# Kernel tuning notes

Hardware: AMD Instinct MI355X
Metric: run time of the kernel (lower is better)

Reference implementation:

```python
import jax, jax.numpy as jnp
import numpy as np

B, S, D = 2, 2048, 512
P, T, MAP_H = 13, 5, 64


def setup_inputs() -> dict:
    key = jax.random.key(0)
    ks = jax.random.split(key, 8)
    s = 0.02
    return {
        "hidden_states": jax.random.normal(ks[0], (B, S, D), jnp.float32),
        "ln_gamma": jnp.ones((D,), jnp.float32),
        "ln_beta": jnp.zeros((D,), jnp.float32),
        "W_in": jax.random.normal(ks[1], (D, P * D), jnp.float32) * s,
        "b_in": jnp.zeros((P * D,), jnp.float32),
        "W_map1": jax.random.normal(ks[2], (D, MAP_H), jnp.float32) * s,
        "b_map1": jnp.zeros((MAP_H,), jnp.float32),
        "W_map2": jax.random.normal(ks[3], (MAP_H, T), jnp.float32) * s,
        "b_map2": jnp.zeros((T,), jnp.float32),
        "log_tau": jnp.linspace(0.0, 4.0, T).astype(jnp.float32),
        "mix": jax.random.normal(ks[4], (P, T), jnp.float32) / float(P * T),
        "W_out": jax.random.normal(ks[5], (D, D), jnp.float32) * s,
        "b_out": jnp.zeros((D,), jnp.float32),
        "scale": jnp.float32(1e-3),
        "h_prev": jnp.zeros((B, P, T, D), jnp.float32),
        "position_offset": 0,
    }


def _forward(hidden_states, ln_gamma, ln_beta, W_in, b_in, W_map1, b_map1,
             W_map2, b_map2, log_tau, mix, W_out, b_out, scale, h_prev):
    b, s_len, d = hidden_states.shape
    p, t = mix.shape
    # pre-norm (LayerNorm, eps=1e-5)
    mu = jnp.mean(hidden_states, -1, keepdims=True)
    var = jnp.var(hidden_states, -1, keepdims=True)
    xn = (hidden_states - mu) * jax.lax.rsqrt(var + 1e-5) * ln_gamma + ln_beta
    # per-protofilament input drive: [B,S,P,D]
    u = (xn @ W_in + b_in).reshape(b, s_len, p, d)
    # liquid (input-dependent) decay per time scale: [B,S,T]
    gate = jax.nn.sigmoid(jnp.tanh(xn @ W_map1 + b_map1) @ W_map2 + b_map2)
    alpha = jnp.exp(-gate / jnp.exp(log_tau))  # [B,S,T]

    def step(h, inp):
        u_t, a_t = inp                      # [B,P,D], [B,T]
        a = a_t[:, None, :, None]           # broadcast over P and D
        h = a * h + (1.0 - a) * u_t[:, :, None, :]   # [B,P,T,D]
        y = jnp.einsum('bptd,pt->bd', h, mix)        # mix protofilaments/time scales
        return h, y

    _, ys = jax.lax.scan(step, h_prev,
                         (jnp.moveaxis(u, 1, 0), jnp.moveaxis(alpha, 1, 0)))
    mt_out = jnp.moveaxis(ys, 0, 1) @ W_out + b_out  # [B,S,D]
    return hidden_states + scale * mt_out


def reference(hidden_states, ln_gamma, ln_beta, W_in, b_in, W_map1, b_map1,
              W_map2, b_map2, log_tau, mix, W_out, b_out, scale, h_prev,
              position_offset):
    return _forward(hidden_states, ln_gamma, ln_beta, W_in, b_in, W_map1,
                    b_map1, W_map2, b_map2, log_tau, mix, W_out, b_out,
                    scale, h_prev)
```

## Files before the change

kernel.cpp:

```cpp
#include <hip/hip_runtime.h>
#include <hip/hip_bf16.h>
#include <stdint.h>

#define BB 2
#define SS 2048
#define DD 512
#define PP 13
#define TT 5
#define MH 64
#define MM (BB*SS)
#define NV (TT*DD)
#define KK 512
#define CHUNK 16
#define NCH (SS/CHUNK)

typedef __attribute__((ext_vector_type(4))) float f32x4;
typedef __attribute__((ext_vector_type(8))) short s8v;
typedef unsigned int u32;
typedef __attribute__((address_space(3))) u32 lds_u32_t;
typedef __attribute__((address_space(1))) const u32 glb_u32_t;

__device__ __forceinline__ float bf2f(unsigned short u){
  union { unsigned int i; float f; } c; c.i = ((unsigned int)u) << 16; return c.f;
}
__device__ __forceinline__ unsigned short f2bf(float f){
  union { float f; unsigned int i; } c; c.f = f;
  unsigned int x = c.i;
  unsigned int r = (x + 0x7fffu + ((x >> 16) & 1u)) >> 16;
  return (unsigned short)r;
}
__device__ __forceinline__ void gld16(unsigned short* l, const unsigned short* g){
  __builtin_amdgcn_global_load_lds((glb_u32_t*)g, (lds_u32_t*)l, 16, 0, 0);
}

__global__ __launch_bounds__(256) void k_prep(
    const float* __restrict__ W_in, const float* __restrict__ b_in,
    const float* __restrict__ mix,  const float* __restrict__ W_out,
    const float* __restrict__ W1,
    unsigned short* __restrict__ W_vT, float* __restrict__ b_v,
    unsigned short* __restrict__ W_outT, unsigned short* __restrict__ W1T)
{
  int blk = blockIdx.x;
  if (blk < 128){
    int idx = blk * 256 + threadIdx.x;
    int d  = idx & (DD-1);
    int k0 = idx >> 9;
    float mx[PP][TT];
    #pragma unroll
    for (int p=0;p<PP;++p)
      #pragma unroll
      for (int t=0;t<TT;++t) mx[p][t] = mix[p*TT+t];
    float acc[TT][8];
    #pragma unroll
    for (int t=0;t<TT;++t)
      #pragma unroll
      for (int j=0;j<8;++j) acc[t][j] = 0.f;
    #pragma unroll
    for (int j=0;j<8;++j){
      int k = k0*8 + j;
      const float* wrow = W_in + (size_t)k * (PP*DD) + d;
      #pragma unroll
      for (int p=0;p<PP;++p){
        float w = wrow[p*DD];
        #pragma unroll
        for (int t=0;t<TT;++t) acc[t][j] += mx[p][t]*w;
      }
    }
    #pragma unroll
    for (int t=0;t<TT;++t){
      union { unsigned short us[8]; uint4 u; } pk;
      #pragma unroll
      for (int j=0;j<8;++j) pk.us[j] = f2bf(acc[t][j]);
      *(uint4*)(W_vT + ((size_t)(t*DD+d))*KK + k0*8) = pk.u;
    }
    if (k0 == 0){
      #pragma unroll
      for (int t=0;t<TT;++t){
        float s = 0.f;
        #pragma unroll
        for (int p=0;p<PP;++p) s += mx[p][t]*b_in[p*DD+d];
        b_v[t*DD+d] = s;
      }
    }
  } else if (blk < 256){
    int idx = (blk-128)*256 + threadIdx.x;
    int n  = idx & (DD-1);
    int k0 = idx >> 9;
    union { unsigned short us[8]; uint4 u; } pk;
    #pragma unroll
    for (int j=0;j<8;++j) pk.us[j] = f2bf(W_out[(size_t)(k0*8+j)*DD + n]);
    *(uint4*)(W_outT + (size_t)n*KK + k0*8) = pk.u;
  } else {
    int idx = (blk-256)*256 + threadIdx.x;
    int n  = idx >> 6;
    int k0 = idx & 63;
    union { unsigned short us[8]; uint4 u; } pk;
    #pragma unroll
    for (int j=0;j<8;++j) pk.us[j] = f2bf(W1[(size_t)(k0*8+j)*MH + n]);
    *(uint4*)(W1T + (size_t)n*KK + k0*8) = pk.u;
  }
}

__global__ __launch_bounds__(256) void k_ln(
    const float* __restrict__ hs,
    const float* __restrict__ gamma, const float* __restrict__ beta,
    unsigned short* __restrict__ xn_bf)
{
  int tid = threadIdx.x;
  int lane = tid & 63;
  int row = blockIdx.x*4 + (tid>>6);
  const float* x = hs + (size_t)row*DD + lane*8;
  float4 v0 = *(const float4*)x;
  float4 v1 = *(const float4*)(x+4);
  float s  = v0.x+v0.y+v0.z+v0.w + v1.x+v1.y+v1.z+v1.w;
  float sq = v0.x*v0.x+v0.y*v0.y+v0.z*v0.z+v0.w*v0.w
           + v1.x*v1.x+v1.y*v1.y+v1.z*v1.z+v1.w*v1.w;
  #pragma unroll
  for (int o=32;o>0;o>>=1){ s += __shfl_xor(s,o); sq += __shfl_xor(sq,o); }
  float mu   = s  * (1.f/DD);
  float var  = sq * (1.f/DD) - mu*mu;
  float rstd = rsqrtf(var + 1e-5f);
  float4 g0 = *(const float4*)(gamma + lane*8);
  float4 g1 = *(const float4*)(gamma + lane*8 + 4);
  float4 b0 = *(const float4*)(beta  + lane*8);
  float4 b1 = *(const float4*)(beta  + lane*8 + 4);
  union { unsigned short us[8]; uint4 u; } pk;
  pk.us[0] = f2bf((v0.x-mu)*rstd*g0.x + b0.x);
  pk.us[1] = f2bf((v0.y-mu)*rstd*g0.y + b0.y);
  pk.us[2] = f2bf((v0.z-mu)*rstd*g0.z + b0.z);
  pk.us[3] = f2bf((v0.w-mu)*rstd*g0.w + b0.w);
  pk.us[4] = f2bf((v1.x-mu)*rstd*g1.x + b1.x);
  pk.us[5] = f2bf((v1.y-mu)*rstd*g1.y + b1.y);
  pk.us[6] = f2bf((v1.z-mu)*rstd*g1.z + b1.z);
  pk.us[7] = f2bf((v1.w-mu)*rstd*g1.w + b1.w);
  *(uint4*)(xn_bf + (size_t)row*DD + lane*8) = pk.u;
}

__global__ __launch_bounds__(256) void k_gate(
    const unsigned short* __restrict__ xn,
    const unsigned short* __restrict__ W1T,
    const float* __restrict__ b1, const float* __restrict__ W2,
    const float* __restrict__ b2, const float* __restrict__ ltau,
    float* __restrict__ alpha)
{
  __shared__ unsigned short lA[2][64*32];
  __shared__ unsigned short lB[2][64*32];
  int bm = blockIdx.x;
  int tid = threadIdx.x, lane = tid & 63, w = tid >> 6;
  int lr = lane & 15, kq = lane >> 4;
  const uint8_t* gA = (const uint8_t*)(xn  + (size_t)(bm*64 + w*16 + (lane>>2))*KK) + (lane&3)*16;
  const uint8_t* gB = (const uint8_t*)(W1T + (size_t)(        w*16 + (lane>>2))*KK) + (lane&3)*16;
  f32x4 acc[4];
  #pragma unroll
  for (int ni=0;ni<4;++ni) acc[ni] = (f32x4){0.f,0.f,0.f,0.f};

  auto stage = [&](int buf, int kt){
    int off = kt*64;
    gld16(&lA[buf][(w*16)*32], (const unsigned short*)(gA + off));
    gld16(&lB[buf][(w*16)*32], (const unsigned short*)(gB + off));
  };
  auto compute = [&](int buf){
    union { uint4 u; s8v v; } af, bfr[4];
    af.u = *(const uint4*)&lA[buf][(w*16+lr)*32 + kq*8];
    #pragma unroll
    for (int ni=0;ni<4;++ni) bfr[ni].u = *(const uint4*)&lB[buf][(ni*16+lr)*32 + kq*8];
    #pragma unroll
    for (int ni=0;ni<4;++ni)
      acc[ni] = __builtin_amdgcn_mfma_f32_16x16x32_bf16(af.v, bfr[ni].v, acc[ni], 0,0,0);
  };

  stage(0, 0);
  __syncthreads();
  #pragma unroll
  for (int kt=1; kt<16; ++kt){
    stage(kt&1, kt);
    compute((kt&1)^1);
    __syncthreads();
  }
  compute(1);

  float z1[4][4];
  #pragma unroll
  for (int ni=0;ni<4;++ni){
    float bb = b1[ni*16+lr];
    #pragma unroll
    for (int r=0;r<4;++r) z1[r][ni] = tanhf(acc[ni][r] + bb);
  }
  float et[TT];
  #pragma unroll
  for (int t=0;t<TT;++t) et[t] = expf(-ltau[t]);
  float a[4][TT];
  #pragma unroll
  for (int t=0;t<TT;++t){
    float w2[4];
    #pragma unroll
    for (int ni=0;ni<4;++ni) w2[ni] = W2[(ni*16+lr)*TT + t];
    #pragma unroll
    for (int r=0;r<4;++r){
      float p = z1[r][0]*w2[0] + z1[r][1]*w2[1] + z1[r][2]*w2[2] + z1[r][3]*w2[3];
      #pragma unroll
      for (int o=8;o>0;o>>=1) p += __shfl_xor(p, o);
      float z2 = p + b2[t];
      float gate = 1.f/(1.f + expf(-z2));
      a[r][t] = expf(-gate * et[t]);
    }
  }
  if (lr < TT){
    int t = lr;
    #pragma unroll
    for (int r=0;r<4;++r){
      int row = bm*64 + w*16 + kq*4 + r;
      alpha[(size_t)row*TT + t] = a[r][t];
    }
  }
}

template<int BN, int NDIM, bool OUTEPI>
__global__ __launch_bounds__(256) void k_gemm(
    const unsigned short* __restrict__ A,
    const unsigned short* __restrict__ Bt,
    const float* __restrict__ bias,
    const float* __restrict__ hidden,
    const float* __restrict__ scale_p,
    float* __restrict__ outF,
    unsigned short* __restrict__ outBf)
{
  constexpr int NI  = (BN == 128) ? 4 : 2;
  constexpr int WNT = BN / 2;
  __shared__ unsigned short lA[2][128*32];
  __shared__ unsigned short lB[2][BN*32];
  int bn = blockIdx.x, bm = blockIdx.y;
  int tid  = threadIdx.x;
  int lane = tid & 63;
  int w    = tid >> 6;
  int wm = w >> 1, wn = w & 1;
  f32x4 acc[4][NI];
  #pragma unroll
  for (int i=0;i<4;++i)
    #pragma unroll
    for (int j=0;j<NI;++j) acc[i][j] = (f32x4){0.f,0.f,0.f,0.f};

  const uint8_t* gA = (const uint8_t*)(A + (size_t)(bm*128 + w*32 + (lane>>2))*KK) + (lane&3)*16;
  const uint8_t* gB;
  if constexpr (BN == 128) gB = (const uint8_t*)(Bt + (size_t)(bn*BN + w*32 + (lane>>2))*KK) + (lane&3)*16;
  else                     gB = (const uint8_t*)(Bt + (size_t)(bn*BN + w*16 + (lane>>2))*KK) + (lane&3)*16;
  int lr = lane & 15, kq = lane >> 4;

  auto stage = [&](int buf, int kt){
    int off = kt*64;
    gld16(&lA[buf][(w*32)*32],    (const unsigned short*)(gA + off));
    gld16(&lA[buf][(w*32+16)*32], (const unsigned short*)(gA + (size_t)16*KK*2 + off));
    if constexpr (BN == 128){
      gld16(&lB[buf][(w*32)*32],    (const unsigned short*)(gB + off));
      gld16(&lB[buf][(w*32+16)*32], (const unsigned short*)(gB + (size_t)16*KK*2 + off));
    } else {
      gld16(&lB[buf][(w*16)*32],    (const unsigned short*)(gB + off));
    }
  };
  auto compute = [&](int buf){
    union { uint4 u; s8v v; } af[4], bfr[NI];
    #pragma unroll
    for (int mi=0;mi<4;++mi) af[mi].u  = *(const uint4*)&lA[buf][(wm*64+mi*16+lr)*32 + kq*8];
    #pragma unroll
    for (int ni=0;ni<NI;++ni) bfr[ni].u = *(const uint4*)&lB[buf][(wn*WNT+ni*16+lr)*32 + kq*8];
    #pragma unroll
    for (int mi=0;mi<4;++mi)
      #pragma unroll
      for (int ni=0;ni<NI;++ni)
        acc[mi][ni] = __builtin_amdgcn_mfma_f32_16x16x32_bf16(af[mi].v, bfr[ni].v, acc[mi][ni], 0,0,0);
  };

  stage(0, 0);
  __syncthreads();
  #pragma unroll
  for (int kt=1; kt<16; ++kt){
    stage(kt&1, kt);
    compute((kt&1)^1);
    __syncthreads();
  }
  compute(1);

  float sc = 0.f;
  if constexpr (OUTEPI) sc = *scale_p;
  #pragma unroll
  for (int mi=0;mi<4;++mi){
    #pragma unroll
    for (int ni=0;ni<NI;++ni){
      int row = bm*128 + wm*64 + mi*16 + kq*4;
      int col = bn*BN  + wn*WNT + ni*16 + lr;
      float bs = bias[col];
      f32x4 c = acc[mi][ni];
      #pragma unroll
      for (int r=0;r<4;++r){
        float val = c[r] + bs;
        size_t off = (size_t)(row+r)*NDIM + col;
        if constexpr (OUTEPI) outF[off] = hidden[off] + sc*val;
        else                  outBf[off] = f2bf(val);
      }
    }
  }
}

__global__ __launch_bounds__(256) void k_scan_a(
    const float* __restrict__ alpha,
    const unsigned short* __restrict__ vg,
    float* __restrict__ L, float* __restrict__ PA)
{
  int blk = blockIdx.x;
  int c = blk % NCH, b = blk / NCH;
  int tid = threadIdx.x;
  __shared__ float sAl[CHUNK*TT];
  if (tid < CHUNK*TT) sAl[tid] = alpha[(size_t)(b*SS + c*CHUNK)*TT + tid];
  __syncthreads();
  float g[TT][2];
  #pragma unroll
  for (int t=0;t<TT;++t){ g[t][0]=0.f; g[t][1]=0.f; }
  const unsigned short* vp = vg + (size_t)(b*SS + c*CHUNK)*NV + tid*2;
  #pragma unroll
  for (int s2=0;s2<CHUNK;++s2){
    #pragma unroll
    for (int t=0;t<TT;++t){
      float a = sAl[s2*TT+t], om = 1.f - a;
      ushort2 vv = *(const ushort2*)(vp + (size_t)s2*NV + t*DD);
      g[t][0] = a*g[t][0] + om*bf2f(vv.x);
      g[t][1] = a*g[t][1] + om*bf2f(vv.y);
    }
  }
  #pragma unroll
  for (int t=0;t<TT;++t){
    float2 o; o.x = g[t][0]; o.y = g[t][1];
    *(float2*)(L + ((size_t)(b*TT+t)*NCH + c)*DD + tid*2) = o;
  }
  if (tid < TT){
    float pa = 1.f;
    #pragma unroll
    for (int s2=0;s2<CHUNK;++s2) pa *= sAl[s2*TT+tid];
    PA[(size_t)(b*TT+tid)*NCH + c] = pa;
  }
}

__global__ __launch_bounds__(512) void k_scan_b(
    const float* __restrict__ mix,
    const float* __restrict__ h_prev,
    const float* __restrict__ PA,
    const float* __restrict__ L,
    float* __restrict__ Gc)
{
  int blk = blockIdx.x;
  int t = blk % TT, b = blk / TT;
  int d = threadIdx.x;
  __shared__ float sP[NCH];
  if (d < NCH) sP[d] = PA[(size_t)(b*TT+t)*NCH + d];
  __syncthreads();
  float carry = 0.f;
  #pragma unroll
  for (int p=0;p<PP;++p)
    carry += mix[p*TT+t] * h_prev[((size_t)(b*PP+p)*TT + t)*DD + d];
  const float* Lp = L  + (size_t)(b*TT+t)*NCH*DD + d;
  float*       gc = Gc + (size_t)(b*TT+t)*NCH*DD + d;
  float buf[8], nbuf[8];
  #pragma unroll
  for (int j=0;j<8;++j) buf[j] = Lp[(size_t)j*DD];
  for (int c0=0;c0<NCH;c0+=8){
    if (c0+8 < NCH){
      #pragma unroll
      for (int j=0;j<8;++j) nbuf[j] = Lp[(size_t)(c0+8+j)*DD];
    }
    #pragma unroll
    for (int j=0;j<8;++j){
      gc[(size_t)(c0+j)*DD] = carry;
      carry = sP[c0+j]*carry + buf[j];
    }
    #pragma unroll
    for (int j=0;j<8;++j) buf[j] = nbuf[j];
  }
}

__global__ __launch_bounds__(256) void k_scan_c(
    const float* __restrict__ alpha,
    const unsigned short* __restrict__ vg,
    const float* __restrict__ Gc,
    unsigned short* __restrict__ ybf)
{
  int blk = blockIdx.x;
  int c = blk % NCH, b = blk / NCH;
  int tid = threadIdx.x;
  __shared__ float sAl[CHUNK*TT];
  if (tid < CHUNK*TT) sAl[tid] = alpha[(size_t)(b*SS + c*CHUNK)*TT + tid];
  __syncthreads();
  float g[TT][2];
  #pragma unroll
  for (int t=0;t<TT;++t){
    float2 cv = *(const float2*)(Gc + ((size_t)(b*TT+t)*NCH + c)*DD + tid*2);
    g[t][0] = cv.x; g[t][1] = cv.y;
  }
  const unsigned short* vp = vg + (size_t)(b*SS + c*CHUNK)*NV + tid*2;
  unsigned short* yp = ybf + (size_t)(b*SS + c*CHUNK)*DD + tid*2;
  #pragma unroll
  for (int s2=0;s2<CHUNK;++s2){
    float y0 = 0.f, y1 = 0.f;
    #pragma unroll
    for (int t=0;t<TT;++t){
      float a = sAl[s2*TT+t], om = 1.f - a;
      ushort2 vv = *(const ushort2*)(vp + (size_t)s2*NV + t*DD);
      g[t][0] = a*g[t][0] + om*bf2f(vv.x);
      g[t][1] = a*g[t][1] + om*bf2f(vv.y);
      y0 += g[t][0]; y1 += g[t][1];
    }
    ushort2 o; o.x = f2bf(y0); o.y = f2bf(y1);
    *(ushort2*)(yp + (size_t)s2*DD) = o;
  }
}

extern "C" void kernel_launch(void* const* d_in, const int* in_sizes, int n_in,
                              void* d_out, int out_size, void* d_ws, size_t ws_size,
                              hipStream_t stream)
{
  (void)in_sizes; (void)n_in; (void)out_size; (void)ws_size;
  const float* hs     = (const float*)d_in[0];
  const float* gamma  = (const float*)d_in[1];
  const float* beta   = (const float*)d_in[2];
  const float* W_in   = (const float*)d_in[3];
  const float* b_in   = (const float*)d_in[4];
  const float* W1     = (const float*)d_in[5];
  const float* b1     = (const float*)d_in[6];
  const float* W2     = (const float*)d_in[7];
  const float* b2     = (const float*)d_in[8];
  const float* ltau   = (const float*)d_in[9];
  const float* mix    = (const float*)d_in[10];
  const float* W_out  = (const float*)d_in[11];
  const float* b_out  = (const float*)d_in[12];
  const float* scale  = (const float*)d_in[13];
  const float* h_prev = (const float*)d_in[14];
  float* out = (float*)d_out;

  uint8_t* w = (uint8_t*)d_ws;
  unsigned short* xn   = (unsigned short*)(w);
  unsigned short* WvT  = (unsigned short*)(w + 4194304);
  unsigned short* WoT  = (unsigned short*)(w + 6815744);
  float* alpha         = (float*)(w + 7340032);
  float* b_v           = (float*)(w + 7421952);
  float* PA            = (float*)(w + 7432192);
  float* L             = (float*)(w + 7437312);
  float* Gc            = (float*)(w + 10058752);
  unsigned short* vg   = (unsigned short*)(w + 12680192);
  unsigned short* ybf  = (unsigned short*)(w + 33651712);
  unsigned short* W1T  = ybf;

  hipLaunchKernelGGL(k_prep, dim3(272), dim3(256), 0, stream,
                     W_in, b_in, mix, W_out, W1, WvT, b_v, WoT, W1T);
  hipLaunchKernelGGL(k_ln,   dim3(MM/4), dim3(256), 0, stream, hs, gamma, beta, xn);
  hipLaunchKernelGGL(k_gate, dim3(MM/64), dim3(256), 0, stream, xn, W1T, b1, W2, b2, ltau, alpha);
  hipLaunchKernelGGL((k_gemm<128,NV,false>), dim3(NV/128, MM/128), dim3(256), 0, stream,
                     xn, WvT, b_v, nullptr, nullptr, nullptr, vg);
  hipLaunchKernelGGL(k_scan_a, dim3(BB*NCH), dim3(256), 0, stream, alpha, vg, L, PA);
  hipLaunchKernelGGL(k_scan_b, dim3(BB*TT), dim3(512), 0, stream, mix, h_prev, PA, L, Gc);
  hipLaunchKernelGGL(k_scan_c, dim3(BB*NCH), dim3(256), 0, stream, alpha, vg, Gc, ybf);
  hipLaunchKernelGGL((k_gemm<64,DD,true>), dim3(DD/64, MM/128), dim3(256), 0, stream,
                     ybf, WoT, b_out, hs, scale, out, nullptr);
}
```

Before: 85.33 us.

## Fuse chunked scan phases into one cooperative kernel and merge LayerNorm into prep

Merges the three scan kernels into one cooperative kernel that uses grid-wide syncs between the local chunk scan, the cross-chunk carry scan and the final output pass. Each thread keeps its local per-step outputs in registers and adds the carry contribution as a cumulative decay product, so vg is not re-read in the last phase. LayerNorm is folded into the weight-prep kernel to save a launch. The cost is register pressure from the held chunk outputs, plus grid.sync overhead and a carry phase that runs on only 20 blocks while the rest wait.

```diff
diff --git a/kernel.cpp b/kernel.cpp
--- a/kernel.cpp
+++ b/kernel.cpp
@@ -1,6 +1,9 @@
 #include <hip/hip_runtime.h>
 #include <hip/hip_bf16.h>
+#include <hip/hip_cooperative_groups.h>
 #include <stdint.h>
+
+namespace cg = cooperative_groups;
 
 #define BB 2
 #define SS 2048
@@ -33,16 +36,48 @@
   __builtin_amdgcn_global_load_lds((glb_u32_t*)g, (lds_u32_t*)l, 16, 0, 0);
 }
 
-__global__ __launch_bounds__(256) void k_prep(
+__global__ __launch_bounds__(256) void k_prep_ln(
+    const float* __restrict__ hs,
+    const float* __restrict__ gamma, const float* __restrict__ beta,
     const float* __restrict__ W_in, const float* __restrict__ b_in,
     const float* __restrict__ mix,  const float* __restrict__ W_out,
     const float* __restrict__ W1,
+    unsigned short* __restrict__ xn_bf,
     unsigned short* __restrict__ W_vT, float* __restrict__ b_v,
     unsigned short* __restrict__ W_outT, unsigned short* __restrict__ W1T)
 {
   int blk = blockIdx.x;
-  if (blk < 128){
-    int idx = blk * 256 + threadIdx.x;
+  if (blk < 1024){
+    int tid = threadIdx.x;
+    int lane = tid & 63;
+    int row = blk*4 + (tid>>6);
+    const float* x = hs + (size_t)row*DD + lane*8;
+    float4 v0 = *(const float4*)x;
+    float4 v1 = *(const float4*)(x+4);
+    float s  = v0.x+v0.y+v0.z+v0.w + v1.x+v1.y+v1.z+v1.w;
+    float sq = v0.x*v0.x+v0.y*v0.y+v0.z*v0.z+v0.w*v0.w
+             + v1.x*v1.x+v1.y*v1.y+v1.z*v1.z+v1.w*v1.w;
+    #pragma unroll
+    for (int o=32;o>0;o>>=1){ s += __shfl_xor(s,o); sq += __shfl_xor(sq,o); }
+    float mu   = s  * (1.f/DD);
+    float var  = sq * (1.f/DD) - mu*mu;
+    float rstd = rsqrtf(var + 1e-5f);
+    float4 g0 = *(const float4*)(gamma + lane*8);
+    float4 g1 = *(const float4*)(gamma + lane*8 + 4);
+    float4 b0 = *(const float4*)(beta  + lane*8);
+    float4 b1 = *(const float4*)(beta  + lane*8 + 4);
+    union { unsigned short us[8]; uint4 u; } pk;
+    pk.us[0] = f2bf((v0.x-mu)*rstd*g0.x + b0.x);
+    pk.us[1] = f2bf((v0.y-mu)*rstd*g0.y + b0.y);
+    pk.us[2] = f2bf((v0.z-mu)*rstd*g0.z + b0.z);
+    pk.us[3] = f2bf((v0.w-mu)*rstd*g0.w + b0.w);
+    pk.us[4] = f2bf((v1.x-mu)*rstd*g1.x + b1.x);
+    pk.us[5] = f2bf((v1.y-mu)*rstd*g1.y + b1.y);
+    pk.us[6] = f2bf((v1.z-mu)*rstd*g1.z + b1.z);
+    pk.us[7] = f2bf((v1.w-mu)*rstd*g1.w + b1.w);
+    *(uint4*)(xn_bf + (size_t)row*DD + lane*8) = pk.u;
+  } else if (blk < 1152){
+    int idx = (blk-1024) * 256 + threadIdx.x;
     int d  = idx & (DD-1);
     int k0 = idx >> 9;
     float mx[PP][TT];
@@ -82,8 +117,8 @@
         b_v[t*DD+d] = s;
       }
     }
-  } else if (blk < 256){
-    int idx = (blk-128)*256 + threadIdx.x;
+  } else if (blk < 1280){
+    int idx = (blk-1152)*256 + threadIdx.x;
     int n  = idx & (DD-1);
     int k0 = idx >> 9;
     union { unsigned short us[8]; uint4 u; } pk;
@@ -91,7 +126,7 @@
     for (int j=0;j<8;++j) pk.us[j] = f2bf(W_out[(size_t)(k0*8+j)*DD + n]);
     *(uint4*)(W_outT + (size_t)n*KK + k0*8) = pk.u;
   } else {
-    int idx = (blk-256)*256 + threadIdx.x;
+    int idx = (blk-1280)*256 + threadIdx.x;
     int n  = idx >> 6;
     int k0 = idx & 63;
     union { unsigned short us[8]; uint4 u; } pk;
@@ -99,41 +134,6 @@
     for (int j=0;j<8;++j) pk.us[j] = f2bf(W1[(size_t)(k0*8+j)*MH + n]);
     *(uint4*)(W1T + (size_t)n*KK + k0*8) = pk.u;
   }
-}
-
-__global__ __launch_bounds__(256) void k_ln(
-    const float* __restrict__ hs,
-    const float* __restrict__ gamma, const float* __restrict__ beta,
-    unsigned short* __restrict__ xn_bf)
-{
-  int tid = threadIdx.x;
-  int lane = tid & 63;
-  int row = blockIdx.x*4 + (tid>>6);
-  const float* x = hs + (size_t)row*DD + lane*8;
-  float4 v0 = *(const float4*)x;
-  float4 v1 = *(const float4*)(x+4);
-  float s  = v0.x+v0.y+v0.z+v0.w + v1.x+v1.y+v1.z+v1.w;
-  float sq = v0.x*v0.x+v0.y*v0.y+v0.z*v0.z+v0.w*v0.w
-           + v1.x*v1.x+v1.y*v1.y+v1.z*v1.z+v1.w*v1.w;
-  #pragma unroll
-  for (int o=32;o>0;o>>=1){ s += __shfl_xor(s,o); sq += __shfl_xor(sq,o); }
-  float mu   = s  * (1.f/DD);
-  float var  = sq * (1.f/DD) - mu*mu;
-  float rstd = rsqrtf(var + 1e-5f);
-  float4 g0 = *(const float4*)(gamma + lane*8);
-  float4 g1 = *(const float4*)(gamma + lane*8 + 4);
-  float4 b0 = *(const float4*)(beta  + lane*8);
-  float4 b1 = *(const float4*)(beta  + lane*8 + 4);
-  union { unsigned short us[8]; uint4 u; } pk;
-  pk.us[0] = f2bf((v0.x-mu)*rstd*g0.x + b0.x);
-  pk.us[1] = f2bf((v0.y-mu)*rstd*g0.y + b0.y);
-  pk.us[2] = f2bf((v0.z-mu)*rstd*g0.z + b0.z);
-  pk.us[3] = f2bf((v0.w-mu)*rstd*g0.w + b0.w);
-  pk.us[4] = f2bf((v1.x-mu)*rstd*g1.x + b1.x);
-  pk.us[5] = f2bf((v1.y-mu)*rstd*g1.y + b1.y);
-  pk.us[6] = f2bf((v1.z-mu)*rstd*g1.z + b1.z);
-  pk.us[7] = f2bf((v1.w-mu)*rstd*g1.w + b1.w);
-  *(uint4*)(xn_bf + (size_t)row*DD + lane*8) = pk.u;
 }
 
 __global__ __launch_bounds__(256) void k_gate(
@@ -301,34 +301,44 @@
   }
 }
 
-__global__ __launch_bounds__(256) void k_scan_a(
+__global__ __launch_bounds__(256) void k_scan(
     const float* __restrict__ alpha,
     const unsigned short* __restrict__ vg,
-    float* __restrict__ L, float* __restrict__ PA)
+    const float* __restrict__ mix,
+    const float* __restrict__ h_prev,
+    float* __restrict__ L, float* __restrict__ PA,
+    float* __restrict__ Gc, unsigned short* __restrict__ ybf)
 {
+  cg::grid_group grid = cg::this_grid();
   int blk = blockIdx.x;
-  int c = blk % NCH, b = blk / NCH;
+  int c = blk & (NCH-1), b = blk >> 7;
   int tid = threadIdx.x;
   __shared__ float sAl[CHUNK*TT];
+  __shared__ float sP[NCH];
   if (tid < CHUNK*TT) sAl[tid] = alpha[(size_t)(b*SS + c*CHUNK)*TT + tid];
   __syncthreads();
-  float g[TT][2];
-  #pragma unroll
-  for (int t=0;t<TT;++t){ g[t][0]=0.f; g[t][1]=0.f; }
+
+  float g0[TT], g1[TT];
+  #pragma unroll
+  for (int t=0;t<TT;++t){ g0[t]=0.f; g1[t]=0.f; }
+  float ylo0[CHUNK], ylo1[CHUNK];
   const unsigned short* vp = vg + (size_t)(b*SS + c*CHUNK)*NV + tid*2;
   #pragma unroll
   for (int s2=0;s2<CHUNK;++s2){
+    float y0 = 0.f, y1 = 0.f;
     #pragma unroll
     for (int t=0;t<TT;++t){
       float a = sAl[s2*TT+t], om = 1.f - a;
       ushort2 vv = *(const ushort2*)(vp + (size_t)s2*NV + t*DD);
-      g[t][0] = a*g[t][0] + om*bf2f(vv.x);
-      g[t][1] = a*g[t][1] + om*bf2f(vv.y);
-    }
+      g0[t] = a*g0[t] + om*bf2f(vv.x);
+      g1[t] = a*g1[t] + om*bf2f(vv.y);
+      y0 += g0[t]; y1 += g1[t];
+    }
+    ylo0[s2] = y0; ylo1[s2] = y1;
   }
   #pragma unroll
   for (int t=0;t<TT;++t){
-    float2 o; o.x = g[t][0]; o.y = g[t][1];
+    float2 o; o.x = g0[t]; o.y = g1[t];
     *(float2*)(L + ((size_t)(b*TT+t)*NCH + c)*DD + tid*2) = o;
   }
   if (tid < TT){
@@ -337,75 +347,56 @@
     for (int s2=0;s2<CHUNK;++s2) pa *= sAl[s2*TT+tid];
     PA[(size_t)(b*TT+tid)*NCH + c] = pa;
   }
-}
-
-__global__ __launch_bounds__(512) void k_scan_b(
-    const float* __restrict__ mix,
-    const float* __restrict__ h_prev,
-    const float* __restrict__ PA,
-    const float* __restrict__ L,
-    float* __restrict__ Gc)
-{
-  int blk = blockIdx.x;
-  int t = blk % TT, b = blk / TT;
-  int d = threadIdx.x;
-  __shared__ float sP[NCH];
-  if (d < NCH) sP[d] = PA[(size_t)(b*TT+t)*NCH + d];
-  __syncthreads();
-  float carry = 0.f;
-  #pragma unroll
-  for (int p=0;p<PP;++p)
-    carry += mix[p*TT+t] * h_prev[((size_t)(b*PP+p)*TT + t)*DD + d];
-  const float* Lp = L  + (size_t)(b*TT+t)*NCH*DD + d;
-  float*       gc = Gc + (size_t)(b*TT+t)*NCH*DD + d;
-  float buf[8], nbuf[8];
-  #pragma unroll
-  for (int j=0;j<8;++j) buf[j] = Lp[(size_t)j*DD];
-  for (int c0=0;c0<NCH;c0+=8){
-    if (c0+8 < NCH){
-      #pragma unroll
-      for (int j=0;j<8;++j) nbuf[j] = Lp[(size_t)(c0+8+j)*DD];
-    }
-    #pragma unroll
-    for (int j=0;j<8;++j){
-      gc[(size_t)(c0+j)*DD] = carry;
-      carry = sP[c0+j]*carry + buf[j];
-    }
-    #pragma unroll
-    for (int j=0;j<8;++j) buf[j] = nbuf[j];
-  }
-}
-
-__global__ __launch_bounds__(256) void k_scan_c(
-    const float* __restrict__ alpha,
-    const unsigned short* __restrict__ vg,
-    const float* __restrict__ Gc,
-    unsigned short* __restrict__ ybf)
-{
-  int blk = blockIdx.x;
-  int c = blk % NCH, b = blk / NCH;
-  int tid = threadIdx.x;
-  __shared__ float sAl[CHUNK*TT];
-  if (tid < CHUNK*TT) sAl[tid] = alpha[(size_t)(b*SS + c*CHUNK)*TT + tid];
-  __syncthreads();
-  float g[TT][2];
+  __threadfence();
+  grid.sync();
+
+  if (blk < 2*BB*TT){
+    int bt = blk >> 1;
+    int t = bt % TT, b2 = bt / TT;
+    int d = (blk & 1)*256 + tid;
+    if (tid < NCH) sP[tid] = PA[(size_t)bt*NCH + tid];
+    __syncthreads();
+    float carry = 0.f;
+    #pragma unroll
+    for (int p=0;p<PP;++p)
+      carry += mix[p*TT+t] * h_prev[((size_t)(b2*PP+p)*TT + t)*DD + d];
+    const float* Lp = L  + (size_t)bt*NCH*DD + d;
+    float*       gc = Gc + (size_t)bt*NCH*DD + d;
+    float buf[8], nbuf[8];
+    #pragma unroll
+    for (int j=0;j<8;++j) buf[j] = Lp[(size_t)j*DD];
+    for (int c0=0;c0<NCH;c0+=8){
+      if (c0+8 < NCH){
+        #pragma unroll
+        for (int j=0;j<8;++j) nbuf[j] = Lp[(size_t)(c0+8+j)*DD];
+      }
+      #pragma unroll
+      for (int j=0;j<8;++j){
+        gc[(size_t)(c0+j)*DD] = carry;
+        carry = sP[c0+j]*carry + buf[j];
+      }
+      #pragma unroll
+      for (int j=0;j<8;++j) buf[j] = nbuf[j];
+    }
+    __threadfence();
+  }
+  grid.sync();
+
+  float ca0[TT], ca1[TT], pr[TT];
   #pragma unroll
   for (int t=0;t<TT;++t){
     float2 cv = *(const float2*)(Gc + ((size_t)(b*TT+t)*NCH + c)*DD + tid*2);
-    g[t][0] = cv.x; g[t][1] = cv.y;
-  }
-  const unsigned short* vp = vg + (size_t)(b*SS + c*CHUNK)*NV + tid*2;
+    ca0[t] = cv.x; ca1[t] = cv.y; pr[t] = 1.f;
+  }
   unsigned short* yp = ybf + (size_t)(b*SS + c*CHUNK)*DD + tid*2;
   #pragma unroll
   for (int s2=0;s2<CHUNK;++s2){
-    float y0 = 0.f, y1 = 0.f;
+    float y0 = ylo0[s2], y1 = ylo1[s2];
     #pragma unroll
     for (int t=0;t<TT;++t){
-      float a = sAl[s2*TT+t], om = 1.f - a;
-      ushort2 vv = *(const ushort2*)(vp + (size_t)s2*NV + t*DD);
-      g[t][0] = a*g[t][0] + om*bf2f(vv.x);
-      g[t][1] = a*g[t][1] + om*bf2f(vv.y);
-      y0 += g[t][0]; y1 += g[t][1];
+      pr[t] *= sAl[s2*TT+t];
+      y0 += pr[t]*ca0[t];
+      y1 += pr[t]*ca1[t];
     }
     ushort2 o; o.x = f2bf(y0); o.y = f2bf(y1);
     *(ushort2*)(yp + (size_t)s2*DD) = o;
@@ -438,7 +429,7 @@
   unsigned short* xn   = (unsigned short*)(w);
   unsigned short* WvT  = (unsigned short*)(w + 4194304);
   unsigned short* WoT  = (unsigned short*)(w + 6815744);
-  float* alpha         = (float*)(w + 7340032);
+  float* alphaB        = (float*)(w + 7340032);
   float* b_v           = (float*)(w + 7421952);
   float* PA            = (float*)(w + 7432192);
   float* L             = (float*)(w + 7437312);
@@ -447,15 +438,20 @@
   unsigned short* ybf  = (unsigned short*)(w + 33651712);
   unsigned short* W1T  = ybf;
 
-  hipLaunchKernelGGL(k_prep, dim3(272), dim3(256), 0, stream,
-                     W_in, b_in, mix, W_out, W1, WvT, b_v, WoT, W1T);
-  hipLaunchKernelGGL(k_ln,   dim3(MM/4), dim3(256), 0, stream, hs, gamma, beta, xn);
-  hipLaunchKernelGGL(k_gate, dim3(MM/64), dim3(256), 0, stream, xn, W1T, b1, W2, b2, ltau, alpha);
+  hipLaunchKernelGGL(k_prep_ln, dim3(1296), dim3(256), 0, stream,
+                     hs, gamma, beta, W_in, b_in, mix, W_out, W1,
+                     xn, WvT, b_v, WoT, W1T);
+  hipLaunchKernelGGL(k_gate, dim3(MM/64), dim3(256), 0, stream, xn, W1T, b1, W2, b2, ltau, alphaB);
   hipLaunchKernelGGL((k_gemm<128,NV,false>), dim3(NV/128, MM/128), dim3(256), 0, stream,
                      xn, WvT, b_v, nullptr, nullptr, nullptr, vg);
-  hipLaunchKernelGGL(k_scan_a, dim3(BB*NCH), dim3(256), 0, stream, alpha, vg, L, PA);
-  hipLaunchKernelGGL(k_scan_b, dim3(BB*TT), dim3(512), 0, stream, mix, h_prev, PA, L, Gc);
-  hipLaunchKernelGGL(k_scan_c, dim3(BB*NCH), dim3(256), 0, stream, alpha, vg, Gc, ybf);
+  {
+    const float* a0 = alphaB; const unsigned short* a1 = vg;
+    const float* a2 = mix; const float* a3 = h_prev;
+    float* a4 = L; float* a5 = PA; float* a6 = Gc; unsigned short* a7 = ybf;
+    void* args[] = { (void*)&a0, (void*)&a1, (void*)&a2, (void*)&a3,
+                     (void*)&a4, (void*)&a5, (void*)&a6, (void*)&a7 };
+    hipLaunchCooperativeKernel((const void*)k_scan, dim3(BB*NCH), dim3(256), args, 0, stream);
+  }
   hipLaunchKernelGGL((k_gemm<64,DD,true>), dim3(DD/64, MM/128), dim3(256), 0, stream,
                      ybf, WoT, b_out, hs, scale, out, nullptr);
 }
```

Measured after the change: 184.8 us. +116.6%, slower.

## Merge LN into prep kernel and parallelize chunk scan over time scales and steps

Applied to the files above, without the earlier changes.

Folds the LayerNorm kernel into the weight-prep launch so one kernel is removed. The chunked scan is restructured: pass A gives each thread one time scale and 8 channels, writes the local prefix states back over vg in bf16, and computes PA per thread. Pass C then reads those stored local states and adds the carried-in state scaled by cumulative decay products, splitting the 16 steps of a chunk across 4 thread groups instead of running them serially. This trades an extra bf16 write of the full vg tensor for more parallelism and wider loads, and rounds the intermediate local states to bf16.

```diff
diff --git a/kernel.cpp b/kernel.cpp
--- a/kernel.cpp
+++ b/kernel.cpp
@@ -33,16 +33,48 @@
   __builtin_amdgcn_global_load_lds((glb_u32_t*)g, (lds_u32_t*)l, 16, 0, 0);
 }
 
-__global__ __launch_bounds__(256) void k_prep(
+__global__ __launch_bounds__(256) void k_prep_ln(
+    const float* __restrict__ hs,
+    const float* __restrict__ gamma, const float* __restrict__ beta,
     const float* __restrict__ W_in, const float* __restrict__ b_in,
     const float* __restrict__ mix,  const float* __restrict__ W_out,
     const float* __restrict__ W1,
+    unsigned short* __restrict__ xn_bf,
     unsigned short* __restrict__ W_vT, float* __restrict__ b_v,
     unsigned short* __restrict__ W_outT, unsigned short* __restrict__ W1T)
 {
   int blk = blockIdx.x;
-  if (blk < 128){
-    int idx = blk * 256 + threadIdx.x;
+  if (blk < 1024){
+    int tid = threadIdx.x;
+    int lane = tid & 63;
+    int row = blk*4 + (tid>>6);
+    const float* x = hs + (size_t)row*DD + lane*8;
+    float4 v0 = *(const float4*)x;
+    float4 v1 = *(const float4*)(x+4);
+    float s  = v0.x+v0.y+v0.z+v0.w + v1.x+v1.y+v1.z+v1.w;
+    float sq = v0.x*v0.x+v0.y*v0.y+v0.z*v0.z+v0.w*v0.w
+             + v1.x*v1.x+v1.y*v1.y+v1.z*v1.z+v1.w*v1.w;
+    #pragma unroll
+    for (int o=32;o>0;o>>=1){ s += __shfl_xor(s,o); sq += __shfl_xor(sq,o); }
+    float mu   = s  * (1.f/DD);
+    float var  = sq * (1.f/DD) - mu*mu;
+    float rstd = rsqrtf(var + 1e-5f);
+    float4 g0 = *(const float4*)(gamma + lane*8);
+    float4 g1 = *(const float4*)(gamma + lane*8 + 4);
+    float4 b0 = *(const float4*)(beta  + lane*8);
+    float4 b1 = *(const float4*)(beta  + lane*8 + 4);
+    union { unsigned short us[8]; uint4 u; } pk;
+    pk.us[0] = f2bf((v0.x-mu)*rstd*g0.x + b0.x);
+    pk.us[1] = f2bf((v0.y-mu)*rstd*g0.y + b0.y);
+    pk.us[2] = f2bf((v0.z-mu)*rstd*g0.z + b0.z);
+    pk.us[3] = f2bf((v0.w-mu)*rstd*g0.w + b0.w);
+    pk.us[4] = f2bf((v1.x-mu)*rstd*g1.x + b1.x);
+    pk.us[5] = f2bf((v1.y-mu)*rstd*g1.y + b1.y);
+    pk.us[6] = f2bf((v1.z-mu)*rstd*g1.z + b1.z);
+    pk.us[7] = f2bf((v1.w-mu)*rstd*g1.w + b1.w);
+    *(uint4*)(xn_bf + (size_t)row*DD + lane*8) = pk.u;
+  } else if (blk < 1152){
+    int idx = (blk-1024) * 256 + threadIdx.x;
     int d  = idx & (DD-1);
     int k0 = idx >> 9;
     float mx[PP][TT];
@@ -82,8 +114,8 @@
         b_v[t*DD+d] = s;
       }
     }
-  } else if (blk < 256){
-    int idx = (blk-128)*256 + threadIdx.x;
+  } else if (blk < 1280){
+    int idx = (blk-1152)*256 + threadIdx.x;
     int n  = idx & (DD-1);
     int k0 = idx >> 9;
     union { unsigned short us[8]; uint4 u; } pk;
@@ -91,7 +123,7 @@
     for (int j=0;j<8;++j) pk.us[j] = f2bf(W_out[(size_t)(k0*8+j)*DD + n]);
     *(uint4*)(W_outT + (size_t)n*KK + k0*8) = pk.u;
   } else {
-    int idx = (blk-256)*256 + threadIdx.x;
+    int idx = (blk-1280)*256 + threadIdx.x;
     int n  = idx >> 6;
     int k0 = idx & 63;
     union { unsigned short us[8]; uint4 u; } pk;
@@ -99,41 +131,6 @@
     for (int j=0;j<8;++j) pk.us[j] = f2bf(W1[(size_t)(k0*8+j)*MH + n]);
     *(uint4*)(W1T + (size_t)n*KK + k0*8) = pk.u;
   }
-}
-
-__global__ __launch_bounds__(256) void k_ln(
-    const float* __restrict__ hs,
-    const float* __restrict__ gamma, const float* __restrict__ beta,
-    unsigned short* __restrict__ xn_bf)
-{
-  int tid = threadIdx.x;
-  int lane = tid & 63;
-  int row = blockIdx.x*4 + (tid>>6);
-  const float* x = hs + (size_t)row*DD + lane*8;
-  float4 v0 = *(const float4*)x;
-  float4 v1 = *(const float4*)(x+4);
-  float s  = v0.x+v0.y+v0.z+v0.w + v1.x+v1.y+v1.z+v1.w;
-  float sq = v0.x*v0.x+v0.y*v0.y+v0.z*v0.z+v0.w*v0.w
-           + v1.x*v1.x+v1.y*v1.y+v1.z*v1.z+v1.w*v1.w;
-  #pragma unroll
-  for (int o=32;o>0;o>>=1){ s += __shfl_xor(s,o); sq += __shfl_xor(sq,o); }
-  float mu   = s  * (1.f/DD);
-  float var  = sq * (1.f/DD) - mu*mu;
-  float rstd = rsqrtf(var + 1e-5f);
-  float4 g0 = *(const float4*)(gamma + lane*8);
-  float4 g1 = *(const float4*)(gamma + lane*8 + 4);
-  float4 b0 = *(const float4*)(beta  + lane*8);
-  float4 b1 = *(const float4*)(beta  + lane*8 + 4);
-  union { unsigned short us[8]; uint4 u; } pk;
-  pk.us[0] = f2bf((v0.x-mu)*rstd*g0.x + b0.x);
-  pk.us[1] = f2bf((v0.y-mu)*rstd*g0.y + b0.y);
-  pk.us[2] = f2bf((v0.z-mu)*rstd*g0.z + b0.z);
-  pk.us[3] = f2bf((v0.w-mu)*rstd*g0.w + b0.w);
-  pk.us[4] = f2bf((v1.x-mu)*rstd*g1.x + b1.x);
-  pk.us[5] = f2bf((v1.y-mu)*rstd*g1.y + b1.y);
-  pk.us[6] = f2bf((v1.z-mu)*rstd*g1.z + b1.z);
-  pk.us[7] = f2bf((v1.w-mu)*rstd*g1.w + b1.w);
-  *(uint4*)(xn_bf + (size_t)row*DD + lane*8) = pk.u;
 }
 
 __global__ __launch_bounds__(256) void k_gate(
@@ -301,42 +298,41 @@
   }
 }
 
-__global__ __launch_bounds__(256) void k_scan_a(
+__global__ __launch_bounds__(320) void k_scan_a(
     const float* __restrict__ alpha,
-    const unsigned short* __restrict__ vg,
+    unsigned short* __restrict__ vg,
     float* __restrict__ L, float* __restrict__ PA)
 {
   int blk = blockIdx.x;
-  int c = blk % NCH, b = blk / NCH;
+  int c = blk & (NCH-1), b = blk >> 7;
   int tid = threadIdx.x;
+  int t  = tid >> 6;
+  int d8 = tid & 63;
   __shared__ float sAl[CHUNK*TT];
   if (tid < CHUNK*TT) sAl[tid] = alpha[(size_t)(b*SS + c*CHUNK)*TT + tid];
   __syncthreads();
-  float g[TT][2];
-  #pragma unroll
-  for (int t=0;t<TT;++t){ g[t][0]=0.f; g[t][1]=0.f; }
-  const unsigned short* vp = vg + (size_t)(b*SS + c*CHUNK)*NV + tid*2;
+  unsigned short* vp = vg + (size_t)(b*SS + c*CHUNK)*NV + t*DD + d8*8;
+  uint4 vv[CHUNK];
+  #pragma unroll
+  for (int s2=0;s2<CHUNK;++s2) vv[s2] = *(const uint4*)(vp + (size_t)s2*NV);
+  float g[8];
+  #pragma unroll
+  for (int j=0;j<8;++j) g[j] = 0.f;
+  float pa = 1.f;
   #pragma unroll
   for (int s2=0;s2<CHUNK;++s2){
-    #pragma unroll
-    for (int t=0;t<TT;++t){
-      float a = sAl[s2*TT+t], om = 1.f - a;
-      ushort2 vv = *(const ushort2*)(vp + (size_t)s2*NV + t*DD);
-      g[t][0] = a*g[t][0] + om*bf2f(vv.x);
-      g[t][1] = a*g[t][1] + om*bf2f(vv.y);
-    }
-  }
-  #pragma unroll
-  for (int t=0;t<TT;++t){
-    float2 o; o.x = g[t][0]; o.y = g[t][1];
-    *(float2*)(L + ((size_t)(b*TT+t)*NCH + c)*DD + tid*2) = o;
-  }
-  if (tid < TT){
-    float pa = 1.f;
-    #pragma unroll
-    for (int s2=0;s2<CHUNK;++s2) pa *= sAl[s2*TT+tid];
-    PA[(size_t)(b*TT+tid)*NCH + c] = pa;
-  }
+    float a = sAl[s2*TT+t], om = 1.f - a;
+    const unsigned short* pv = (const unsigned short*)&vv[s2];
+    union { unsigned short us[8]; uint4 u; } o;
+    #pragma unroll
+    for (int j=0;j<8;++j){ g[j] = a*g[j] + om*bf2f(pv[j]); o.us[j] = f2bf(g[j]); }
+    *(uint4*)(vp + (size_t)s2*NV) = o.u;
+    pa *= a;
+  }
+  float* Lp = L + ((size_t)(b*TT+t)*NCH + c)*DD + d8*8;
+  *(float4*)Lp     = (float4){g[0],g[1],g[2],g[3]};
+  *(float4*)(Lp+4) = (float4){g[4],g[5],g[6],g[7]};
+  if (d8 == 0) PA[(size_t)(b*TT+t)*NCH + c] = pa;
 }
 
 __global__ __launch_bounds__(512) void k_scan_b(
@@ -378,37 +374,54 @@
 
 __global__ __launch_bounds__(256) void k_scan_c(
     const float* __restrict__ alpha,
-    const unsigned short* __restrict__ vg,
+    const unsigned short* __restrict__ g_loc,
     const float* __restrict__ Gc,
     unsigned short* __restrict__ ybf)
 {
   int blk = blockIdx.x;
-  int c = blk % NCH, b = blk / NCH;
+  int c = blk & (NCH-1), b = blk >> 7;
   int tid = threadIdx.x;
+  int s4 = tid >> 6;
+  int d8 = tid & 63;
   __shared__ float sAl[CHUNK*TT];
   if (tid < CHUNK*TT) sAl[tid] = alpha[(size_t)(b*SS + c*CHUNK)*TT + tid];
   __syncthreads();
-  float g[TT][2];
+  float ca[TT][8];
   #pragma unroll
   for (int t=0;t<TT;++t){
-    float2 cv = *(const float2*)(Gc + ((size_t)(b*TT+t)*NCH + c)*DD + tid*2);
-    g[t][0] = cv.x; g[t][1] = cv.y;
-  }
-  const unsigned short* vp = vg + (size_t)(b*SS + c*CHUNK)*NV + tid*2;
-  unsigned short* yp = ybf + (size_t)(b*SS + c*CHUNK)*DD + tid*2;
-  #pragma unroll
-  for (int s2=0;s2<CHUNK;++s2){
-    float y0 = 0.f, y1 = 0.f;
+    const float* gp = Gc + ((size_t)(b*TT+t)*NCH + c)*DD + d8*8;
+    float4 c0 = *(const float4*)gp;
+    float4 c1 = *(const float4*)(gp+4);
+    ca[t][0]=c0.x; ca[t][1]=c0.y; ca[t][2]=c0.z; ca[t][3]=c0.w;
+    ca[t][4]=c1.x; ca[t][5]=c1.y; ca[t][6]=c1.z; ca[t][7]=c1.w;
+  }
+  float pr[TT];
+  #pragma unroll
+  for (int t=0;t<TT;++t){
+    float p = 1.f;
+    for (int j=0;j<s4*4;++j) p *= sAl[j*TT+t];
+    pr[t] = p;
+  }
+  const unsigned short* gl = g_loc + (size_t)(b*SS + c*CHUNK)*NV + d8*8;
+  unsigned short* yp = ybf + (size_t)(b*SS + c*CHUNK)*DD + d8*8;
+  #pragma unroll
+  for (int i=0;i<4;++i){
+    int s2 = s4*4 + i;
+    float y[8];
+    #pragma unroll
+    for (int j=0;j<8;++j) y[j] = 0.f;
     #pragma unroll
     for (int t=0;t<TT;++t){
-      float a = sAl[s2*TT+t], om = 1.f - a;
-      ushort2 vv = *(const ushort2*)(vp + (size_t)s2*NV + t*DD);
-      g[t][0] = a*g[t][0] + om*bf2f(vv.x);
-      g[t][1] = a*g[t][1] + om*bf2f(vv.y);
-      y0 += g[t][0]; y1 += g[t][1];
-    }
-    ushort2 o; o.x = f2bf(y0); o.y = f2bf(y1);
-    *(ushort2*)(yp + (size_t)s2*DD) = o;
+      pr[t] *= sAl[s2*TT+t];
+      uint4 gv = *(const uint4*)(gl + (size_t)s2*NV + t*DD);
+      const unsigned short* gp = (const unsigned short*)&gv;
+      #pragma unroll
+      for (int j=0;j<8;++j) y[j] += bf2f(gp[j]) + pr[t]*ca[t][j];
+    }
+    union { unsigned short us[8]; uint4 u; } o;
+    #pragma unroll
+    for (int j=0;j<8;++j) o.us[j] = f2bf(y[j]);
+    *(uint4*)(yp + (size_t)s2*DD) = o.u;
   }
 }
 
@@ -438,7 +451,7 @@
   unsigned short* xn   = (unsigned short*)(w);
   unsigned short* WvT  = (unsigned short*)(w + 4194304);
   unsigned short* WoT  = (unsigned short*)(w + 6815744);
-  float* alpha         = (float*)(w + 7340032);
+  float* alphaB        = (float*)(w + 7340032);
   float* b_v           = (float*)(w + 7421952);
   float* PA            = (float*)(w + 7432192);
   float* L             = (float*)(w + 7437312);
@@ -447,15 +460,15 @@
   unsigned short* ybf  = (unsigned short*)(w + 33651712);
   unsigned short* W1T  = ybf;
 
-  hipLaunchKernelGGL(k_prep, dim3(272), dim3(256), 0, stream,
-                     W_in, b_in, mix, W_out, W1, WvT, b_v, WoT, W1T);
-  hipLaunchKernelGGL(k_ln,   dim3(MM/4), dim3(256), 0, stream, hs, gamma, beta, xn);
-  hipLaunchKernelGGL(k_gate, dim3(MM/64), dim3(256), 0, stream, xn, W1T, b1, W2, b2, ltau, alpha);
+  hipLaunchKernelGGL(k_prep_ln, dim3(1296), dim3(256), 0, stream,
+                     hs, gamma, beta, W_in, b_in, mix, W_out, W1,
+                     xn, WvT, b_v, WoT, W1T);
+  hipLaunchKernelGGL(k_gate, dim3(MM/64), dim3(256), 0, stream, xn, W1T, b1, W2, b2, ltau, alphaB);
   hipLaunchKernelGGL((k_gemm<128,NV,false>), dim3(NV/128, MM/128), dim3(256), 0, stream,
                      xn, WvT, b_v, nullptr, nullptr, nullptr, vg);
-  hipLaunchKernelGGL(k_scan_a, dim3(BB*NCH), dim3(256), 0, stream, alpha, vg, L, PA);
+  hipLaunchKernelGGL(k_scan_a, dim3(BB*NCH), dim3(320), 0, stream, alphaB, vg, L, PA);
   hipLaunchKernelGGL(k_scan_b, dim3(BB*TT), dim3(512), 0, stream, mix, h_prev, PA, L, Gc);
-  hipLaunchKernelGGL(k_scan_c, dim3(BB*NCH), dim3(256), 0, stream, alpha, vg, Gc, ybf);
+  hipLaunchKernelGGL(k_scan_c, dim3(BB*NCH), dim3(256), 0, stream, alphaB, vg, Gc, ybf);
   hipLaunchKernelGGL((k_gemm<64,DD,true>), dim3(DD/64, MM/128), dim3(256), 0, stream,
                      ybf, WoT, b_out, hs, scale, out, nullptr);
 }
```

After: 82.95 us. -2.8%, faster.
